# Kernel tuning notes

Measured on AMD Instinct MI355X. Metric: run time of the kernel, lower is better.

## Reference

```python
import jax, jax.numpy as jnp
import numpy as np

GRAD_FACTOR = 1.5
TAU = 30.0
K = 16

@jax.custom_vjp
def grad_scale(x):
    return x

def _gs_fwd(x):
    return x, None

def _gs_bwd(_, g):
    return (g * GRAD_FACTOR,)

grad_scale.defvjp(_gs_fwd, _gs_bwd)


def logic_layer(x, idx, w):
    # x: [..., D]; idx: [2, out] int; w: [out, 16]
    # difflogic soft logic layer: softmax over the 16 two-input boolean ops.
    x = grad_scale(x)
    a = x[..., idx[0]]
    b = x[..., idx[1]]
    ab = a * b
    ops = jnp.stack([
        jnp.zeros_like(a),          # 0: FALSE
        ab,                         # 1: a AND b
        a - ab,                     # 2: a AND NOT b
        a,                          # 3: a
        b - ab,                     # 4: NOT a AND b
        b,                          # 5: b
        a + b - 2 * ab,             # 6: XOR
        a + b - ab,                 # 7: OR
        1 - (a + b - ab),           # 8: NOR
        1 - (a + b - 2 * ab),       # 9: XNOR
        1 - b,                      # 10: NOT b
        1 - b + ab,                 # 11: a OR NOT b
        1 - a,                      # 12: NOT a
        1 - a + ab,                 # 13: NOT a OR b
        1 - ab,                     # 14: NAND
        jnp.ones_like(a),           # 15: TRUE
    ], axis=-1)                     # [..., out, 16]
    p = jax.nn.softmax(w, axis=-1)  # [out, 16]
    return jnp.einsum('...ok,ok->...o', ops, p)


def logic_tree(xp, i0, w0, i1, w1, i2, w2):
    # depth-3 tree: in_dim -> 4 -> 2 -> 1
    h = logic_layer(xp, i0, w0)
    h = logic_layer(h, i1, w1)
    h = logic_layer(h, i2, w2)
    return h[..., 0]


def conv(x, params, ksize, stride, pad):
    # per-filter logic-tree conv (unfold + vmapped trees over out_channels)
    B, C, H, W = x.shape
    xp = jnp.pad(x, ((0, 0), (0, 0), (pad, pad), (pad, pad)))
    oh = (H + 2 * pad - ksize) // stride + 1
    ow = (W + 2 * pad - ksize) // stride + 1
    # patches ordered channel-major then (ki, kj), matching F.unfold
    pat = jnp.stack([xp[:, :, i:i + oh * stride:stride, j:j + ow * stride:stride]
                     for i in range(ksize) for j in range(ksize)], axis=2)  # [B,C,k*k,oh,ow]
    pat = pat.reshape(B, C * ksize * ksize, oh * ow).transpose(0, 2, 1)
    pat = pat.reshape(B * oh * ow, C * ksize * ksize)  # [(B*L), C*k*k]
    # vmap over filters: idx [2,F,d], w [F,d,16]
    out = jax.vmap(logic_tree, in_axes=(None, 1, 0, 1, 0, 1, 0))(pat, *params)  # [F, B*L]
    return out.reshape(-1, B, oh, ow).transpose(1, 0, 2, 3)


def orpool(x):
    return jax.lax.reduce_window(x, -jnp.inf, jax.lax.max, (1, 1, 2, 2), (1, 1, 2, 2), 'VALID')


def _tree_params(rng, in_dim, n_filters):
    dims = [(in_dim, 4), (4, 2), (2, 1)]
    out = []
    for d_in, d_out in dims:
        idx = rng.randint(0, d_in, size=(2, n_filters, d_out)).astype(np.int32)
        w = (0.1 * rng.randn(n_filters, d_out, 16)).astype(np.float32)
        w[..., 3] += 5.0  # 'residual' init favors pass-through op
        out += [jnp.asarray(idx), jnp.asarray(w)]
    return out


def _fc_params(rng, d_in, d_out):
    idx = rng.randint(0, d_in, size=(2, d_out)).astype(np.int32)
    w = (0.1 * rng.randn(d_out, 16)).astype(np.float32)
    w[..., 3] += 5.0
    return jnp.asarray(idx), jnp.asarray(w)


def setup_inputs() -> dict:
    key = jax.random.key(0)
    rng = np.random.RandomState(0)
    inp = {"x": jax.random.uniform(key, (100, 1, 28, 28), dtype=jnp.float32)}
    for name, in_dim, f in [("c1", 25, K), ("c2", 9 * K, 3 * K), ("c3", 27 * K, 9 * K)]:
        p = _tree_params(rng, in_dim, f)
        for li in range(3):
            inp[f"{name}_idx{li}"] = p[2 * li]
            inp[f"{name}_w{li}"] = p[2 * li + 1]
    for name, d_in, d_out in [("fc1", 81 * K, 1280 * K), ("fc2", 1280 * K, 640 * K), ("fc3", 640 * K, 320 * K)]:
        idx, w = _fc_params(rng, d_in, d_out)
        inp[f"{name}_idx"] = idx
        inp[f"{name}_w"] = w
    return inp


def reference(x,
              c1_idx0, c1_w0, c1_idx1, c1_w1, c1_idx2, c1_w2,
              c2_idx0, c2_w0, c2_idx1, c2_w1, c2_idx2, c2_w2,
              c3_idx0, c3_w0, c3_idx1, c3_w1, c3_idx2, c3_w2,
              fc1_idx, fc1_w, fc2_idx, fc2_w, fc3_idx, fc3_w):
    x = (x > 0.5).astype(jnp.float32)
    x = conv(x, (c1_idx0, c1_w0, c1_idx1, c1_w1, c1_idx2, c1_w2), 5, 1, 0)
    x = orpool(x)
    x = conv(x, (c2_idx0, c2_w0, c2_idx1, c2_w1, c2_idx2, c2_w2), 3, 1, 1)
    x = orpool(x)
    x = conv(x, (c3_idx0, c3_w0, c3_idx1, c3_w1, c3_idx2, c3_w2), 3, 1, 1)
    x = orpool(x)
    B = x.shape[0]
    x = x.reshape(B, -1)  # [B, 81*K]
    x = logic_layer(x, fc1_idx, fc1_w)
    x = logic_layer(x, fc2_idx, fc2_w)
    x = logic_layer(x, fc3_idx, fc3_w)
    # GroupSum(k=10, tau=30)
    return x.reshape(B, 10, -1).sum(-1) / TAU
```

## Files before the change

### kernel.cpp

```cpp
#include <hip/hip_runtime.h>
#include <hip/hip_fp16.h>
#include <math.h>

#define DEV __device__ __forceinline__

DEV float gev(float4 c, float a, float b) {
    return fmaf(c.w, a * b, fmaf(c.z, b, fmaf(c.y, a, c.x)));
}

DEV float sel4(const float h[4], int i) {
    float r = h[0];
    r = (i == 1) ? h[1] : r;
    r = (i == 2) ? h[2] : r;
    r = (i == 3) ? h[3] : r;
    return r;
}

DEV float sel2(const float h[2], int i) { return (i == 1) ? h[1] : h[0]; }

__global__ __launch_bounds__(256) void coef_kernel(
    const float* __restrict__ w0, const float* __restrict__ w1,
    const float* __restrict__ w2, const float* __restrict__ w3,
    const float* __restrict__ w4, const float* __restrict__ w5,
    const float* __restrict__ w6, const float* __restrict__ w7,
    const float* __restrict__ w8, const float* __restrict__ w9,
    const float* __restrict__ w10, const float* __restrict__ w11,
    float4* __restrict__ coef)
{
    int t = blockIdx.x * 256 + threadIdx.x;
    if (t >= 37296) return;
    const float* wrow;
    if      (t < 64)    wrow = w0  + t * 16;
    else if (t < 96)    wrow = w1  + (t - 64) * 16;
    else if (t < 112)   wrow = w2  + (t - 96) * 16;
    else if (t < 304)   wrow = w3  + (t - 112) * 16;
    else if (t < 400)   wrow = w4  + (t - 304) * 16;
    else if (t < 448)   wrow = w5  + (t - 400) * 16;
    else if (t < 1024)  wrow = w6  + (t - 448) * 16;
    else if (t < 1312)  wrow = w7  + (t - 1024) * 16;
    else if (t < 1456)  wrow = w8  + (t - 1312) * 16;
    else if (t < 21936) wrow = w9  + (t - 1456) * 16;
    else if (t < 32176) wrow = w10 + (t - 21936) * 16;
    else                wrow = w11 + (t - 32176) * 16;

    const float4* wv = (const float4*)wrow;
    float4 q0 = wv[0], q1 = wv[1], q2 = wv[2], q3 = wv[3];
    float p[16] = {q0.x,q0.y,q0.z,q0.w, q1.x,q1.y,q1.z,q1.w,
                   q2.x,q2.y,q2.z,q2.w, q3.x,q3.y,q3.z,q3.w};
    float mx = p[0];
    #pragma unroll
    for (int k = 1; k < 16; k++) mx = fmaxf(mx, p[k]);
    float s = 0.f;
    #pragma unroll
    for (int k = 0; k < 16; k++) { p[k] = __expf(p[k] - mx); s += p[k]; }
    float inv = 1.f / s;
    #pragma unroll
    for (int k = 0; k < 16; k++) p[k] *= inv;

    float c0  = p[8]+p[9]+p[10]+p[11]+p[12]+p[13]+p[14]+p[15];
    float ca  = p[2]+p[3]+p[6]+p[7]-p[8]-p[9]-p[12]-p[13];
    float cb  = p[4]+p[5]+p[6]+p[7]-p[8]-p[9]-p[10]-p[11];
    float cab = p[1]-p[2]-p[4]-2.f*p[6]-p[7]+p[8]+2.f*p[9]+p[11]+p[13]-p[14];
    coef[t] = make_float4(c0, ca, cb, cab);
}

template <int CIN, int KS, int PAD, int HIN, int F>
DEV void conv_stage(const float* Sin, float* Sout,
                    const int* __restrict__ idx0, const int* __restrict__ idx1,
                    const int* __restrict__ idx2,
                    const float4* __restrict__ cf0, const float4* __restrict__ cf1,
                    const float4* __restrict__ cf2, int tid)
{
    constexpr int HP = (HIN + 2 * PAD - KS + 1) / 2;
    for (int t = tid; t < F * HP * HP; t += 1024) {
        int pw = t % HP;
        int ph = (t / HP) % HP;
        int f  = t / (HP * HP);

        int a0[4], b0[4];
        #pragma unroll
        for (int g = 0; g < 4; g++) { a0[g] = idx0[f*4+g]; b0[g] = idx0[F*4 + f*4+g]; }
        int a1[2], b1[2];
        #pragma unroll
        for (int g = 0; g < 2; g++) { a1[g] = idx1[f*2+g]; b1[g] = idx1[F*2 + f*2+g]; }
        int a2 = idx2[f], b2 = idx2[F + f];
        float4 C0[4] = {cf0[f*4], cf0[f*4+1], cf0[f*4+2], cf0[f*4+3]};
        float4 C1[2] = {cf1[f*2], cf1[f*2+1]};
        float4 C2 = cf2[f];

        float m = -1e30f;
        #pragma unroll
        for (int dy = 0; dy < 2; dy++) {
            #pragma unroll
            for (int dx = 0; dx < 2; dx++) {
                int oh = 2 * ph + dy, ow = 2 * pw + dx;
                float va[4], vb[4];
                #pragma unroll
                for (int g = 0; g < 4; g++) {
                    int tt = a0[g];
                    int c = tt / (KS * KS), r = tt % (KS * KS);
                    int y = oh + r / KS - PAD, xx = ow + r % KS - PAD;
                    bool ok = (PAD == 0) || (y >= 0 && y < HIN && xx >= 0 && xx < HIN);
                    va[g] = ok ? Sin[(c * HIN + y) * HIN + xx] : 0.f;
                }
                #pragma unroll
                for (int g = 0; g < 4; g++) {
                    int tt = b0[g];
                    int c = tt / (KS * KS), r = tt % (KS * KS);
                    int y = oh + r / KS - PAD, xx = ow + r % KS - PAD;
                    bool ok = (PAD == 0) || (y >= 0 && y < HIN && xx >= 0 && xx < HIN);
                    vb[g] = ok ? Sin[(c * HIN + y) * HIN + xx] : 0.f;
                }
                float h0[4];
                #pragma unroll
                for (int g = 0; g < 4; g++) h0[g] = gev(C0[g], va[g], vb[g]);
                float h1[2];
                #pragma unroll
                for (int g = 0; g < 2; g++)
                    h1[g] = gev(C1[g], sel4(h0, a1[g]), sel4(h0, b1[g]));
                float v = gev(C2, sel2(h1, a2), sel2(h1, b2));
                m = fmaxf(m, v);
            }
        }
        Sout[t] = m;
    }
}

template <int DOUT, typename TIN, typename TOUT>
DEV void fc_stage(const TIN* Sin, TOUT* Sout, const int* __restrict__ idx,
                  const float4* __restrict__ cf, int tid)
{
    constexpr int K = DOUT / 1024;
    #pragma unroll 1
    for (int k0 = 0; k0 < K; k0 += 5) {
        int ia[5], ib[5];
        float4 c[5];
        #pragma unroll
        for (int j = 0; j < 5; j++) {
            int o = tid + (k0 + j) * 1024;
            ia[j] = idx[o];
            ib[j] = idx[DOUT + o];
            c[j]  = cf[o];
        }
        float va[5], vb[5];
        #pragma unroll
        for (int j = 0; j < 5; j++) {
            va[j] = (float)Sin[ia[j]];
            vb[j] = (float)Sin[ib[j]];
        }
        #pragma unroll
        for (int j = 0; j < 5; j++) {
            int o = tid + (k0 + j) * 1024;
            Sout[o] = (TOUT)gev(c[j], va[j], vb[j]);
        }
    }
}

__global__ __launch_bounds__(1024, 1) void fused_net(
    const float* __restrict__ x,
    const int* __restrict__ c1i0, const int* __restrict__ c1i1, const int* __restrict__ c1i2,
    const int* __restrict__ c2i0, const int* __restrict__ c2i1, const int* __restrict__ c2i2,
    const int* __restrict__ c3i0, const int* __restrict__ c3i1, const int* __restrict__ c3i2,
    const int* __restrict__ fc1i, const int* __restrict__ fc2i, const int* __restrict__ fc3i,
    const float4* __restrict__ coef,
    float* __restrict__ out)
{
    __shared__ __align__(16) char S[65408];
    float*  XB = (float*)S;
    float*  P1 = (float*)S + 784;
    float*  P2 = (float*)S + 3088;
    float*  P3 = (float*)S + 4816;
    __half* F1 = (__half*)(S + 24448);
    __half* F2 = (__half*)(S + 0);
    float*  F3 = (float*)(S + 24448);

    const int b = blockIdx.x, tid = threadIdx.x;
    const float* xb = x + b * 784;
    if (tid < 784) XB[tid] = xb[tid] > 0.5f ? 1.f : 0.f;
    __syncthreads();

    conv_stage<1, 5, 0, 28, 16>(XB, P1, c1i0, c1i1, c1i2,
                                coef + 0, coef + 64, coef + 96, tid);
    __syncthreads();
    conv_stage<16, 3, 1, 12, 48>(P1, P2, c2i0, c2i1, c2i2,
                                 coef + 112, coef + 304, coef + 400, tid);
    __syncthreads();
    conv_stage<48, 3, 1, 6, 144>(P2, P3, c3i0, c3i1, c3i2,
                                 coef + 448, coef + 1024, coef + 1312, tid);
    __syncthreads();

    fc_stage<20480>(P3, F1, fc1i, coef + 1456, tid);
    __syncthreads();
    fc_stage<10240>(F1, F2, fc2i, coef + 21936, tid);
    __syncthreads();
    fc_stage<5120>(F2, F3, fc3i, coef + 32176, tid);
    __syncthreads();

    int wave = tid >> 6, lane = tid & 63;
    if (wave < 10) {
        float s = 0.f;
        #pragma unroll
        for (int i = 0; i < 8; i++) s += F3[wave * 512 + i * 64 + lane];
        #pragma unroll
        for (int off = 32; off > 0; off >>= 1) s += __shfl_down(s, off, 64);
        if (lane == 0) out[b * 10 + wave] = s * (1.f / 30.f);
    }
}

extern "C" void kernel_launch(void* const* d_in, const int* in_sizes, int n_in,
                              void* d_out, int out_size, void* d_ws, size_t ws_size,
                              hipStream_t stream)
{
    const float* x     = (const float*)d_in[0];
    const int*   c1i0  = (const int*)d_in[1];  const float* c1w0 = (const float*)d_in[2];
    const int*   c1i1  = (const int*)d_in[3];  const float* c1w1 = (const float*)d_in[4];
    const int*   c1i2  = (const int*)d_in[5];  const float* c1w2 = (const float*)d_in[6];
    const int*   c2i0  = (const int*)d_in[7];  const float* c2w0 = (const float*)d_in[8];
    const int*   c2i1  = (const int*)d_in[9];  const float* c2w1 = (const float*)d_in[10];
    const int*   c2i2  = (const int*)d_in[11]; const float* c2w2 = (const float*)d_in[12];
    const int*   c3i0  = (const int*)d_in[13]; const float* c3w0 = (const float*)d_in[14];
    const int*   c3i1  = (const int*)d_in[15]; const float* c3w1 = (const float*)d_in[16];
    const int*   c3i2  = (const int*)d_in[17]; const float* c3w2 = (const float*)d_in[18];
    const int*   fc1i  = (const int*)d_in[19]; const float* fc1w = (const float*)d_in[20];
    const int*   fc2i  = (const int*)d_in[21]; const float* fc2w = (const float*)d_in[22];
    const int*   fc3i  = (const int*)d_in[23]; const float* fc3w = (const float*)d_in[24];

    float4* coef = (float4*)d_ws;

    coef_kernel<<<146, 256, 0, stream>>>(
        c1w0, c1w1, c1w2, c2w0, c2w1, c2w2, c3w0, c3w1, c3w2,
        fc1w, fc2w, fc3w, coef);

    fused_net<<<100, 1024, 0, stream>>>(
        x,
        c1i0, c1i1, c1i2, c2i0, c2i1, c2i2, c3i0, c3i1, c3i2,
        fc1i, fc2i, fc3i, coef, (float*)d_out);
}
```

Before: 144.4 us.

## Prepack conv/fc parameters into per-unit records and pad conv planes in LDS

A setup kernel now packs, per FC neuron, the softmax-derived coefficients together with the two input indices into one 32-byte record. Per conv filter it precomputes flattened input offsets, coefficients and one-hot selectors for the inner tree levels. Conv stages write into zero-padded LDS planes, so bounds checks, div/mod index decoding and select chains disappear from the hot loop, and the FC stages make one packed load per neuron. The launch-bounds occupancy hint and the LDS layout also change. The costs are a larger workspace, some extra FMA work for the one-hot selection, and zero-fill passes over the padded buffers.

New measurement: 134.7 us. 1.07x faster.

```diff
diff --git a/kernel.cpp b/kernel.cpp
--- a/kernel.cpp
+++ b/kernel.cpp
@@ -8,41 +8,7 @@
     return fmaf(c.w, a * b, fmaf(c.z, b, fmaf(c.y, a, c.x)));
 }
 
-DEV float sel4(const float h[4], int i) {
-    float r = h[0];
-    r = (i == 1) ? h[1] : r;
-    r = (i == 2) ? h[2] : r;
-    r = (i == 3) ? h[3] : r;
-    return r;
-}
-
-DEV float sel2(const float h[2], int i) { return (i == 1) ? h[1] : h[0]; }
-
-__global__ __launch_bounds__(256) void coef_kernel(
-    const float* __restrict__ w0, const float* __restrict__ w1,
-    const float* __restrict__ w2, const float* __restrict__ w3,
-    const float* __restrict__ w4, const float* __restrict__ w5,
-    const float* __restrict__ w6, const float* __restrict__ w7,
-    const float* __restrict__ w8, const float* __restrict__ w9,
-    const float* __restrict__ w10, const float* __restrict__ w11,
-    float4* __restrict__ coef)
-{
-    int t = blockIdx.x * 256 + threadIdx.x;
-    if (t >= 37296) return;
-    const float* wrow;
-    if      (t < 64)    wrow = w0  + t * 16;
-    else if (t < 96)    wrow = w1  + (t - 64) * 16;
-    else if (t < 112)   wrow = w2  + (t - 96) * 16;
-    else if (t < 304)   wrow = w3  + (t - 112) * 16;
-    else if (t < 400)   wrow = w4  + (t - 304) * 16;
-    else if (t < 448)   wrow = w5  + (t - 400) * 16;
-    else if (t < 1024)  wrow = w6  + (t - 448) * 16;
-    else if (t < 1312)  wrow = w7  + (t - 1024) * 16;
-    else if (t < 1456)  wrow = w8  + (t - 1312) * 16;
-    else if (t < 21936) wrow = w9  + (t - 1456) * 16;
-    else if (t < 32176) wrow = w10 + (t - 21936) * 16;
-    else                wrow = w11 + (t - 32176) * 16;
-
+DEV float4 softmax_coef(const float* __restrict__ wrow) {
     const float4* wv = (const float4*)wrow;
     float4 q0 = wv[0], q1 = wv[1], q2 = wv[2], q3 = wv[3];
     float p[16] = {q0.x,q0.y,q0.z,q0.w, q1.x,q1.y,q1.z,q1.w,
@@ -56,91 +22,138 @@
     float inv = 1.f / s;
     #pragma unroll
     for (int k = 0; k < 16; k++) p[k] *= inv;
-
     float c0  = p[8]+p[9]+p[10]+p[11]+p[12]+p[13]+p[14]+p[15];
     float ca  = p[2]+p[3]+p[6]+p[7]-p[8]-p[9]-p[12]-p[13];
     float cb  = p[4]+p[5]+p[6]+p[7]-p[8]-p[9]-p[10]-p[11];
     float cab = p[1]-p[2]-p[4]-2.f*p[6]-p[7]+p[8]+2.f*p[9]+p[11]+p[13]-p[14];
-    coef[t] = make_float4(c0, ca, cb, cab);
-}
-
-template <int CIN, int KS, int PAD, int HIN, int F>
-DEV void conv_stage(const float* Sin, float* Sout,
-                    const int* __restrict__ idx0, const int* __restrict__ idx1,
-                    const int* __restrict__ idx2,
-                    const float4* __restrict__ cf0, const float4* __restrict__ cf1,
-                    const float4* __restrict__ cf2, int tid)
-{
-    constexpr int HP = (HIN + 2 * PAD - KS + 1) / 2;
+    return make_float4(c0, ca, cb, cab);
+}
+
+DEV float4 onehot4(int i) {
+    return make_float4(i == 0 ? 1.f : 0.f, i == 1 ? 1.f : 0.f,
+                       i == 2 ? 1.f : 0.f, i == 3 ? 1.f : 0.f);
+}
+
+__global__ __launch_bounds__(256) void setup_kernel(
+    const int* __restrict__ c1i0, const int* __restrict__ c1i1, const int* __restrict__ c1i2,
+    const int* __restrict__ c2i0, const int* __restrict__ c2i1, const int* __restrict__ c2i2,
+    const int* __restrict__ c3i0, const int* __restrict__ c3i1, const int* __restrict__ c3i2,
+    const float* __restrict__ c1w0, const float* __restrict__ c1w1, const float* __restrict__ c1w2,
+    const float* __restrict__ c2w0, const float* __restrict__ c2w1, const float* __restrict__ c2w2,
+    const float* __restrict__ c3w0, const float* __restrict__ c3w1, const float* __restrict__ c3w2,
+    const int* __restrict__ fc1i, const float* __restrict__ fc1w,
+    const int* __restrict__ fc2i, const float* __restrict__ fc2w,
+    const int* __restrict__ fc3i, const float* __restrict__ fc3w,
+    float4* __restrict__ fcp1, float4* __restrict__ fcp2, float4* __restrict__ fcp3,
+    float4* __restrict__ cvp)
+{
+    int t = blockIdx.x * 256 + threadIdx.x;
+    if (t >= 36048) return;
+    if (t < 35840) {
+        const float* w; const int* idx; float4* dst; int o, D;
+        if (t < 20480)      { o = t;         D = 20480; w = fc1w; idx = fc1i; dst = fcp1; }
+        else if (t < 30720) { o = t - 20480; D = 10240; w = fc2w; idx = fc2i; dst = fcp2; }
+        else                { o = t - 30720; D = 5120;  w = fc3w; idx = fc3i; dst = fcp3; }
+        dst[2 * o] = softmax_coef(w + o * 16);
+        int4 ii = make_int4(idx[o], idx[D + o], 0, 0);
+        ((int4*)dst)[2 * o + 1] = ii;
+        return;
+    }
+    int f = t - 35840;
+    const int *i0, *i1, *i2; const float *W0, *W1, *W2;
+    int F, KS, mode, lf;
+    if (f < 16)      { lf = f;      F = 16;  KS = 5; mode = 1;
+                       i0 = c1i0; i1 = c1i1; i2 = c1i2; W0 = c1w0; W1 = c1w1; W2 = c1w2; }
+    else if (f < 64) { lf = f - 16; F = 48;  KS = 3; mode = 2;
+                       i0 = c2i0; i1 = c2i1; i2 = c2i2; W0 = c2w0; W1 = c2w1; W2 = c2w2; }
+    else             { lf = f - 64; F = 144; KS = 3; mode = 3;
+                       i0 = c3i0; i1 = c3i1; i2 = c3i2; W0 = c3w0; W1 = c3w1; W2 = c3w2; }
+    float4* pk = cvp + f * 14;
+    int offs[8];
+    #pragma unroll
+    for (int g = 0; g < 8; g++) {
+        int tt = (g < 4) ? i0[lf * 4 + g] : i0[F * 4 + lf * 4 + (g - 4)];
+        int kk = KS * KS;
+        int c = tt / kk, r = tt - c * kk;
+        int dy = r / KS, dx = r - dy * KS;
+        int off;
+        if (mode == 1)      off = dy * 28 + dx;
+        else if (mode == 2) off = (c * 14 + dy) * 14 + dx;
+        else                off = (c * 8 + dy) * 8 + dx;
+        offs[g] = off;
+    }
+    ((int4*)pk)[0] = make_int4(offs[0], offs[1], offs[2], offs[3]);
+    ((int4*)pk)[1] = make_int4(offs[4], offs[5], offs[6], offs[7]);
+    #pragma unroll
+    for (int g = 0; g < 4; g++) pk[2 + g] = softmax_coef(W0 + (lf * 4 + g) * 16);
+    int a10 = i1[lf * 2 + 0], a11 = i1[lf * 2 + 1];
+    int b10 = i1[F * 2 + lf * 2 + 0], b11 = i1[F * 2 + lf * 2 + 1];
+    pk[6] = onehot4(a10); pk[7] = onehot4(b10);
+    pk[8] = onehot4(a11); pk[9] = onehot4(b11);
+    pk[10] = softmax_coef(W1 + (lf * 2 + 0) * 16);
+    pk[11] = softmax_coef(W1 + (lf * 2 + 1) * 16);
+    int a2 = i2[lf], b2 = i2[F + lf];
+    pk[12] = make_float4(a2 == 0 ? 1.f : 0.f, a2 == 1 ? 1.f : 0.f,
+                         b2 == 0 ? 1.f : 0.f, b2 == 1 ? 1.f : 0.f);
+    pk[13] = softmax_coef(W2 + lf * 16);
+}
+
+template <int PITCH, int HP, int F, int OUTP>
+DEV void conv_stage(const float* Sin, float* Sout, const float4* __restrict__ pack,
+                    int tid)
+{
     for (int t = tid; t < F * HP * HP; t += 1024) {
-        int pw = t % HP;
-        int ph = (t / HP) % HP;
         int f  = t / (HP * HP);
-
-        int a0[4], b0[4];
-        #pragma unroll
-        for (int g = 0; g < 4; g++) { a0[g] = idx0[f*4+g]; b0[g] = idx0[F*4 + f*4+g]; }
-        int a1[2], b1[2];
-        #pragma unroll
-        for (int g = 0; g < 2; g++) { a1[g] = idx1[f*2+g]; b1[g] = idx1[F*2 + f*2+g]; }
-        int a2 = idx2[f], b2 = idx2[F + f];
-        float4 C0[4] = {cf0[f*4], cf0[f*4+1], cf0[f*4+2], cf0[f*4+3]};
-        float4 C1[2] = {cf1[f*2], cf1[f*2+1]};
-        float4 C2 = cf2[f];
-
+        int p  = t - f * (HP * HP);
+        int ph = p / HP, pw = p - ph * HP;
+        const float4* pk = pack + f * 14;
+        int4 ao = ((const int4*)pk)[0];
+        int4 bo = ((const int4*)pk)[1];
+        float4 C00 = pk[2], C01 = pk[3], C02 = pk[4], C03 = pk[5];
+        float4 oA0 = pk[6], oB0 = pk[7], oA1 = pk[8], oB1 = pk[9];
+        float4 C10 = pk[10], C11 = pk[11], S2 = pk[12], C2 = pk[13];
         float m = -1e30f;
         #pragma unroll
         for (int dy = 0; dy < 2; dy++) {
             #pragma unroll
             for (int dx = 0; dx < 2; dx++) {
-                int oh = 2 * ph + dy, ow = 2 * pw + dx;
-                float va[4], vb[4];
-                #pragma unroll
-                for (int g = 0; g < 4; g++) {
-                    int tt = a0[g];
-                    int c = tt / (KS * KS), r = tt % (KS * KS);
-                    int y = oh + r / KS - PAD, xx = ow + r % KS - PAD;
-                    bool ok = (PAD == 0) || (y >= 0 && y < HIN && xx >= 0 && xx < HIN);
-                    va[g] = ok ? Sin[(c * HIN + y) * HIN + xx] : 0.f;
-                }
-                #pragma unroll
-                for (int g = 0; g < 4; g++) {
-                    int tt = b0[g];
-                    int c = tt / (KS * KS), r = tt % (KS * KS);
-                    int y = oh + r / KS - PAD, xx = ow + r % KS - PAD;
-                    bool ok = (PAD == 0) || (y >= 0 && y < HIN && xx >= 0 && xx < HIN);
-                    vb[g] = ok ? Sin[(c * HIN + y) * HIN + xx] : 0.f;
-                }
-                float h0[4];
-                #pragma unroll
-                for (int g = 0; g < 4; g++) h0[g] = gev(C0[g], va[g], vb[g]);
-                float h1[2];
-                #pragma unroll
-                for (int g = 0; g < 2; g++)
-                    h1[g] = gev(C1[g], sel4(h0, a1[g]), sel4(h0, b1[g]));
-                float v = gev(C2, sel2(h1, a2), sel2(h1, b2));
+                int poff = (2 * ph + dy) * PITCH + (2 * pw + dx);
+                float h00 = gev(C00, Sin[ao.x + poff], Sin[bo.x + poff]);
+                float h01 = gev(C01, Sin[ao.y + poff], Sin[bo.y + poff]);
+                float h02 = gev(C02, Sin[ao.z + poff], Sin[bo.z + poff]);
+                float h03 = gev(C03, Sin[ao.w + poff], Sin[bo.w + poff]);
+                float sa0 = fmaf(oA0.x, h00, fmaf(oA0.y, h01, fmaf(oA0.z, h02, oA0.w * h03)));
+                float sb0 = fmaf(oB0.x, h00, fmaf(oB0.y, h01, fmaf(oB0.z, h02, oB0.w * h03)));
+                float sa1 = fmaf(oA1.x, h00, fmaf(oA1.y, h01, fmaf(oA1.z, h02, oA1.w * h03)));
+                float sb1 = fmaf(oB1.x, h00, fmaf(oB1.y, h01, fmaf(oB1.z, h02, oB1.w * h03)));
+                float h10 = gev(C10, sa0, sb0);
+                float h11 = gev(C11, sa1, sb1);
+                float sa2 = fmaf(S2.x, h10, S2.y * h11);
+                float sb2 = fmaf(S2.z, h10, S2.w * h11);
+                float v = gev(C2, sa2, sb2);
                 m = fmaxf(m, v);
             }
         }
-        Sout[t] = m;
+        if (OUTP)
+            Sout[(f * OUTP + ph + 1) * OUTP + (pw + 1)] = m;
+        else
+            Sout[t] = m;
     }
 }
 
 template <int DOUT, typename TIN, typename TOUT>
-DEV void fc_stage(const TIN* Sin, TOUT* Sout, const int* __restrict__ idx,
-                  const float4* __restrict__ cf, int tid)
+DEV void fc_stage(const TIN* Sin, TOUT* Sout, const float4* __restrict__ pk, int tid)
 {
     constexpr int K = DOUT / 1024;
     #pragma unroll 1
     for (int k0 = 0; k0 < K; k0 += 5) {
-        int ia[5], ib[5];
-        float4 c[5];
+        float4 c[5]; int ia[5], ib[5];
         #pragma unroll
         for (int j = 0; j < 5; j++) {
             int o = tid + (k0 + j) * 1024;
-            ia[j] = idx[o];
-            ib[j] = idx[DOUT + o];
-            c[j]  = cf[o];
+            c[j] = pk[2 * o];
+            int4 ii = ((const int4*)pk)[2 * o + 1];
+            ia[j] = ii.x; ib[j] = ii.y;
         }
         float va[5], vb[5];
         #pragma unroll
@@ -156,44 +169,39 @@
     }
 }
 
-__global__ __launch_bounds__(1024, 1) void fused_net(
+__global__ __launch_bounds__(1024, 4) void fused_net(
     const float* __restrict__ x,
-    const int* __restrict__ c1i0, const int* __restrict__ c1i1, const int* __restrict__ c1i2,
-    const int* __restrict__ c2i0, const int* __restrict__ c2i1, const int* __restrict__ c2i2,
-    const int* __restrict__ c3i0, const int* __restrict__ c3i1, const int* __restrict__ c3i2,
-    const int* __restrict__ fc1i, const int* __restrict__ fc2i, const int* __restrict__ fc3i,
-    const float4* __restrict__ coef,
+    const float4* __restrict__ fcp1, const float4* __restrict__ fcp2,
+    const float4* __restrict__ fcp3, const float4* __restrict__ cvp,
     float* __restrict__ out)
 {
-    __shared__ __align__(16) char S[65408];
-    float*  XB = (float*)S;
-    float*  P1 = (float*)S + 784;
-    float*  P2 = (float*)S + 3088;
-    float*  P3 = (float*)S + 4816;
-    __half* F1 = (__half*)(S + 24448);
-    __half* F2 = (__half*)(S + 0);
-    float*  F3 = (float*)(S + 24448);
+    __shared__ __align__(16) char S[61440];
+    __half* F1h = (__half*)S;
+    __half* F2h = (__half*)(S + 40960);
+    float*  P1p = (float*)S;
+    float*  XB  = (float*)(S + 12544);
+    float*  P2p = (float*)(S + 40960);
+    float*  P3  = (float*)(S + 53248);
+    float*  F3  = (float*)S;
 
     const int b = blockIdx.x, tid = threadIdx.x;
-    const float* xb = x + b * 784;
-    if (tid < 784) XB[tid] = xb[tid] > 0.5f ? 1.f : 0.f;
-    __syncthreads();
-
-    conv_stage<1, 5, 0, 28, 16>(XB, P1, c1i0, c1i1, c1i2,
-                                coef + 0, coef + 64, coef + 96, tid);
-    __syncthreads();
-    conv_stage<16, 3, 1, 12, 48>(P1, P2, c2i0, c2i1, c2i2,
-                                 coef + 112, coef + 304, coef + 400, tid);
-    __syncthreads();
-    conv_stage<48, 3, 1, 6, 144>(P2, P3, c3i0, c3i1, c3i2,
-                                 coef + 448, coef + 1024, coef + 1312, tid);
-    __syncthreads();
-
-    fc_stage<20480>(P3, F1, fc1i, coef + 1456, tid);
-    __syncthreads();
-    fc_stage<10240>(F1, F2, fc2i, coef + 21936, tid);
-    __syncthreads();
-    fc_stage<5120>(F2, F3, fc3i, coef + 32176, tid);
+    if (tid < 784) XB[tid] = x[b * 784 + tid] > 0.5f ? 1.f : 0.f;
+    for (int i = tid; i < 3136; i += 1024) P1p[i] = 0.f;
+    for (int i = tid; i < 3072; i += 1024) P2p[i] = 0.f;
+    __syncthreads();
+
+    conv_stage<28, 12, 16, 14>(XB, P1p, cvp + 0 * 14, tid);
+    __syncthreads();
+    conv_stage<14, 6, 48, 8>(P1p, P2p, cvp + 16 * 14, tid);
+    __syncthreads();
+    conv_stage<8, 3, 144, 0>(P2p, P3, cvp + 64 * 14, tid);
+    __syncthreads();
+
+    fc_stage<20480, float, __half>(P3, F1h, fcp1, tid);
+    __syncthreads();
+    fc_stage<10240, __half, __half>(F1h, F2h, fcp2, tid);
+    __syncthreads();
+    fc_stage<5120, __half, float>(F2h, F3, fcp3, tid);
     __syncthreads();
 
     int wave = tid >> 6, lane = tid & 63;
@@ -225,14 +233,18 @@
     const int*   fc2i  = (const int*)d_in[21]; const float* fc2w = (const float*)d_in[22];
     const int*   fc3i  = (const int*)d_in[23]; const float* fc3w = (const float*)d_in[24];
 
-    float4* coef = (float4*)d_ws;
-
-    coef_kernel<<<146, 256, 0, stream>>>(
+    char* ws = (char*)d_ws;
+    float4* fcp1 = (float4*)ws;
+    float4* fcp2 = (float4*)(ws + 655360);
+    float4* fcp3 = (float4*)(ws + 983040);
+    float4* cvp  = (float4*)(ws + 1146880);
+
+    setup_kernel<<<141, 256, 0, stream>>>(
+        c1i0, c1i1, c1i2, c2i0, c2i1, c2i2, c3i0, c3i1, c3i2,
         c1w0, c1w1, c1w2, c2w0, c2w1, c2w2, c3w0, c3w1, c3w2,
-        fc1w, fc2w, fc3w, coef);
+        fc1i, fc1w, fc2i, fc2w, fc3i, fc3w,
+        fcp1, fcp2, fcp3, cvp);
 
     fused_net<<<100, 1024, 0, stream>>>(
-        x,
-        c1i0, c1i1, c1i2, c2i0, c2i1, c2i2, c3i0, c3i1, c3i2,
-        fc1i, fc2i, fc3i, coef, (float*)d_out);
-}
+        x, fcp1, fcp2, fcp3, cvp, (float*)d_out);
+}
```
